# Kernel optimization log

Hardware: AMD Instinct MI355X
Metric: run time of the kernel (lower is better)

Reference implementation:

```python
import jax, jax.numpy as jnp
import numpy as np

NCHAR, NHID, NSTACK, STACK, DEPTH, T = 256, 2048, 32, 512, 4, 4096
TOP = 0  # top_of_stack


def _xavier(k, shape):
    fan_in, fan_out = shape[-1], shape[-2]
    std = (2.0 / (fan_in + fan_out)) ** 0.5
    return (jax.random.normal(k, shape) * std).astype(jnp.float32)


def setup_inputs() -> dict:
    key = jax.random.key(0)
    ks = jax.random.split(key, 7)
    in2hid_w = _xavier(ks[0], (NHID, NCHAR))
    hid2hid_w = _xavier(ks[1], (NHID, NHID))  # mod=2 -> xavier, not zeros
    hid2act_w = _xavier(ks[2], (NSTACK, 3, NHID))
    # init zero-masks: hid2stack rows below TOP+1 kept, rest zero; stack2hid cols >= DEPTH zero
    hid2stack_w = _xavier(ks[3], (NSTACK, STACK, NHID)).at[:, TOP + 1:, :].set(0.0)
    stack2hid_w = _xavier(ks[4], (NSTACK, NHID, STACK)).at[:, :, TOP + DEPTH:].set(0.0)
    hid2out_w = _xavier(ks[5], (NCHAR, NHID))
    tokens = jax.random.randint(ks[6], (T,), 0, NCHAR, dtype=jnp.int32)
    return dict(tokens=tokens, in2hid_w=in2hid_w, hid2hid_w=hid2hid_w,
                hid2act_w=hid2act_w, hid2stack_w=hid2stack_w,
                stack2hid_w=stack2hid_w, hid2out_w=hid2out_w)


def reference(tokens, in2hid_w, hid2hid_w, hid2act_w, hid2stack_w, stack2hid_w, hid2out_w):
    """Sequential StackRNN (mod=2, use_noop=True, soft actions) over T tokens.
    Shift-matrix matmuls replaced by equivalent O(n) rolls (push/pop/noop
    matrices with TOP=0 are exactly shift-down / shift-up / identity).
    Returns per-step output probabilities [T, NCHAR]."""
    neg_one_col = jnp.full((NSTACK, 1), -1.0, jnp.float32)

    def step(carry, x_t):
        hidden, stacks = carry  # [NHID], [NSTACK, STACK]
        # h = U x_t + sum_s P_s s_{t-1}[:depth] + R h_{t-1}
        h = in2hid_w[:, x_t]
        h = h + jnp.einsum('snd,sd->n', stack2hid_w[:, :, TOP:TOP + DEPTH],
                           stacks[:, TOP:TOP + DEPTH])
        h = h + hid2hid_w @ hidden
        h = jax.nn.sigmoid(h)
        # per-stack action distribution: [pop, push, noop]
        acts = jax.nn.softmax(jnp.einsum('san,n->sa', hid2act_w, h), axis=-1)
        pop_w, push_w, noop_w = acts[:, 0:1], acts[:, 1:2], acts[:, 2:3]
        # pushed top value (only row TOP of hid2stack is used)
        top_val = jax.nn.sigmoid(jnp.clip(hid2stack_w[:, TOP, :] @ h, -50.0, 50.0))  # [NSTACK]
        pushed = jnp.concatenate([top_val[:, None], stacks[:, :-1]], axis=1)
        popped = jnp.concatenate([stacks[:, 1:], neg_one_col], axis=1)
        new_stacks = push_w * pushed + pop_w * popped + noop_w * stacks
        probs = jax.nn.softmax(hid2out_w @ h)
        return (h, new_stacks), probs

    hidden0 = jnp.zeros((NHID,), jnp.float32)
    stacks0 = jnp.full((NSTACK, STACK), -1.0, jnp.float32)
    _, out = jax.lax.scan(step, (hidden0, stacks0), tokens)
    return out  # [T, NCHAR]
```

## Files before the change

kernel.cpp:

```cpp
#include <hip/hip_runtime.h>
#include <math.h>

#define NCHAR 256
#define NHID 2048
#define NSTACK 32
#define STACK 512
#define T 4096
#define NB 64
#define BT 1024
#define RPB 32
#define PROW 128
#define FPAD 16
#define AGENT __HIP_MEMORY_SCOPE_AGENT

__device__ __forceinline__ float cohLoadF(const float* p) {
  return __hip_atomic_load(p, __ATOMIC_RELAXED, AGENT);
}
__device__ __forceinline__ void cohStoreF(float* p, float v) {
  __hip_atomic_store(p, v, __ATOMIC_RELAXED, AGENT);
}
__device__ __forceinline__ float4 cohLoad4(const float4* p) {
  float4 r;
  asm volatile("global_load_dwordx4 %0, %1, off sc0 sc1\n\ts_waitcnt vmcnt(0)"
               : "=&v"(r) : "v"(p) : "memory");
  return r;
}
__device__ __forceinline__ void cohLoad4x4(const float4* p0, const float4* p1,
                                           const float4* p2, const float4* p3,
                                           float4& r0, float4& r1,
                                           float4& r2, float4& r3) {
  asm volatile(
      "global_load_dwordx4 %0, %4, off sc0 sc1\n\t"
      "global_load_dwordx4 %1, %5, off sc0 sc1\n\t"
      "global_load_dwordx4 %2, %6, off sc0 sc1\n\t"
      "global_load_dwordx4 %3, %7, off sc0 sc1\n\t"
      "s_waitcnt vmcnt(0)"
      : "=&v"(r0), "=&v"(r1), "=&v"(r2), "=&v"(r3)
      : "v"(p0), "v"(p1), "v"(p2), "v"(p3)
      : "memory");
}

__global__ __launch_bounds__(BT, 4) void stackrnn_seq(
    const int* __restrict__ tokens,
    const float* __restrict__ in2hid,
    const float* __restrict__ hid2hid,
    const float* __restrict__ hid2act,
    const float* __restrict__ hid2stack,
    const float* __restrict__ stack2hid,
    const float* __restrict__ hid2out,
    float* __restrict__ out,
    float* __restrict__ Hbuf,
    float* __restrict__ Pbuf,
    float* __restrict__ TopsG,
    int*   __restrict__ flags)
{
  __shared__ int    sTok[T];
  __shared__ float4 sH[576];
  __shared__ float4 sPq[32][17];
  __shared__ float  sLl[16][128];
  __shared__ float  sSt[2][STACK];
  __shared__ float  sHnew[RPB];
  __shared__ float  sActs[NSTACK][3];
  __shared__ float  sTopv[NSTACK];
  __shared__ float  sTops[NSTACK][4];
  __shared__ float  sOut[16];

  const int tid = threadIdx.x;
  const int b   = blockIdx.x;
  const int wv  = tid >> 6;
  const int l   = tid & 63;
  const int r0  = b * RPB + 2 * wv;
  const int r1  = r0 + 1;

  float wA[32], wB[32];
  {
    const float4* pa = (const float4*)(hid2hid + (size_t)r0 * NHID + 32 * l);
    const float4* pb = (const float4*)(hid2hid + (size_t)r1 * NHID + 32 * l);
#pragma unroll
    for (int j = 0; j < 8; ++j) {
      float4 v = pa[j];
      wA[4*j] = v.x; wA[4*j+1] = v.y; wA[4*j+2] = v.z; wA[4*j+3] = v.w;
    }
#pragma unroll
    for (int j = 0; j < 8; ++j) {
      float4 v = pb[j];
      wB[4*j] = v.x; wB[4*j+1] = v.y; wB[4*j+2] = v.z; wB[4*j+3] = v.w;
    }
  }
  float wl00, wl01, wl10, wl11;
  {
    const int g0 = 2 * l, g1 = 2 * l + 1;
    const int s0 = g0 >> 2, k0 = g0 & 3, s1 = g1 >> 2, k1 = g1 & 3;
    const float* p0 = (k0 < 3) ? (hid2act + (size_t)(3 * s0 + k0) * NHID)
                               : (hid2stack + (size_t)s0 * STACK * NHID);
    const float* p1 = (k1 < 3) ? (hid2act + (size_t)(3 * s1 + k1) * NHID)
                               : (hid2stack + (size_t)s1 * STACK * NHID);
    wl00 = p0[r0]; wl01 = p0[r1];
    wl10 = p1[r0]; wl11 = p1[r1];
  }
  const int cs = l >> 1, cd = (l & 1) * 2;
  float w2a0, w2a1, w2b0, w2b1;
  {
    const float* p = stack2hid + (size_t)cs * NHID * STACK;
    w2a0 = p[(size_t)r0 * STACK + cd]; w2a1 = p[(size_t)r0 * STACK + cd + 1];
    w2b0 = p[(size_t)r1 * STACK + cd]; w2b1 = p[(size_t)r1 * STACK + cd + 1];
  }
  const int oseg = wv >> 2;
  float wo[8];
  {
    const int ocol = 4 * b + (wv & 3);
    const float4* p = (const float4*)(hid2out + (size_t)ocol * NHID + oseg * 512 + 8 * l);
    float4 v0 = p[0], v1 = p[1];
    wo[0] = v0.x; wo[1] = v0.y; wo[2] = v0.z; wo[3] = v0.w;
    wo[4] = v1.x; wo[5] = v1.y; wo[6] = v1.z; wo[7] = v1.w;
  }

  for (int i = tid; i < T; i += BT) sTok[i] = tokens[i];
  float bval = -1.f;

  __syncthreads();

#pragma unroll 1
  for (int w = 0; w < T; ++w) {
    const int pw_ = w & 1, pr_ = pw_ ^ 1;
    const int xt  = sTok[w];
    const float e0 = in2hid[(size_t)r0 * NCHAR + xt];
    const float e1 = in2hid[(size_t)r1 * NCHAR + xt];

    if (w > 0 && wv == 0) {
      int v;
      do {
        v = __hip_atomic_load(&flags[l * FPAD], __ATOMIC_RELAXED, AGENT);
      } while (__any(v < w));
    }
    __syncthreads();

    float tg0 = -1.f, tg1 = -1.f, tg2 = -1.f, tg3 = -1.f, tg4 = -1.f;
    if (w > 0) {
      if (tid >= 512) {
        const int u = tid - 512;
        float4 hv = cohLoad4((const float4*)(Hbuf + (size_t)pr_ * NHID) + u);
        sH[u + (u >> 3)] = hv;
      } else {
        const int q = tid >> 4, bg = tid & 15;
        const float* base = Pbuf + (size_t)pr_ * NB * PROW + (size_t)(4 * bg) * PROW + 4 * q;
        float4 a0, a1, a2, a3;
        cohLoad4x4((const float4*)base, (const float4*)(base + PROW),
                   (const float4*)(base + 2 * PROW), (const float4*)(base + 3 * PROW),
                   a0, a1, a2, a3);
        float4 s4;
        s4.x = a0.x + a1.x + a2.x + a3.x;
        s4.y = a0.y + a1.y + a2.y + a3.y;
        s4.z = a0.z + a1.z + a2.z + a3.z;
        s4.w = a0.w + a1.w + a2.w + a3.w;
        sPq[q][bg] = s4;
        if (tid < NSTACK) {
          const float* tp = TopsG + ((size_t)pr_ * NSTACK + tid) * 16;
          tg0 = cohLoadF(tp);     tg1 = cohLoadF(tp + 1); tg2 = cohLoadF(tp + 2);
          tg3 = cohLoadF(tp + 3); tg4 = cohLoadF(tp + 4);
        }
      }
    }
    __syncthreads();

    if (tid < NSTACK) {
      if (w > 0) {
        float4 a = make_float4(0.f, 0.f, 0.f, 0.f);
#pragma unroll
        for (int g = 0; g < 16; ++g) {
          const float4 p = sPq[tid][(g + tid) & 15];
          a.x += p.x; a.y += p.y; a.z += p.z; a.w += p.w;
        }
        const float m  = fmaxf(a.x, fmaxf(a.y, a.z));
        const float ea = expf(a.x - m), eb = expf(a.y - m), ec = expf(a.z - m);
        const float inv = 1.f / (ea + eb + ec);
        const float qw = ea * inv, pwt = eb * inv, nw = ec * inv;
        sActs[tid][0] = qw; sActs[tid][1] = pwt; sActs[tid][2] = nw;
        float tv = fminf(50.f, fmaxf(-50.f, a.w));
        tv = 1.f / (1.f + expf(-tv));
        sTopv[tid] = tv;
        sTops[tid][0] = pwt * tv  + qw * tg1 + nw * tg0;
        sTops[tid][1] = pwt * tg0 + qw * tg2 + nw * tg1;
        sTops[tid][2] = pwt * tg1 + qw * tg3 + nw * tg2;
        sTops[tid][3] = pwt * tg2 + qw * tg4 + nw * tg3;
      } else {
        sActs[tid][0] = sActs[tid][1] = sActs[tid][2] = 0.f;
        sTopv[tid] = 0.f;
        sTops[tid][0] = sTops[tid][1] = sTops[tid][2] = sTops[tid][3] = -1.f;
      }
    }
    float acc0 = 0.f, acc1 = 0.f;
    if (w > 0) {
#pragma unroll
      for (int j = 0; j < 8; ++j) {
        const float4 hv = sH[9 * l + j];
        acc0 += wA[4*j]*hv.x + wA[4*j+1]*hv.y + wA[4*j+2]*hv.z + wA[4*j+3]*hv.w;
        acc1 += wB[4*j]*hv.x + wB[4*j+1]*hv.y + wB[4*j+2]*hv.z + wB[4*j+3]*hv.w;
      }
    }
    __syncthreads();

    acc0 += w2a0 * sTops[cs][cd] + w2a1 * sTops[cs][cd + 1];
    acc1 += w2b0 * sTops[cs][cd] + w2b1 * sTops[cs][cd + 1];
#pragma unroll
    for (int m = 1; m < 64; m <<= 1) {
      acc0 += __shfl_xor(acc0, m);
      acc1 += __shfl_xor(acc1, m);
    }
    const float h0 = 1.f / (1.f + expf(-(acc0 + e0)));
    const float h1 = 1.f / (1.f + expf(-(acc1 + e1)));
    if (l == 0) { sHnew[2 * wv] = h0; sHnew[2 * wv + 1] = h1; }
    *(float2*)&sLl[wv][2 * l] =
        make_float2(wl00 * h0 + wl01 * h1, wl10 * h0 + wl11 * h1);

    if (b < NSTACK && tid >= 512) {
      const int d = tid - 512;
      float nv;
      if (w > 0) {
        const float left   = (d > 0) ? sSt[pr_][d - 1] : 0.f;
        const float pushed = (d == 0) ? sTopv[b] : left;
        const float popped = (d < STACK - 1) ? sSt[pr_][d + 1] : -1.f;
        nv = sActs[b][1] * pushed + sActs[b][0] * popped + sActs[b][2] * bval;
      } else {
        nv = -1.f;
      }
      bval = nv;
      sSt[pw_][d] = nv;
      if (d < 5) cohStoreF(&TopsG[((size_t)pw_ * NSTACK + b) * 16 + d], nv);
    }
    if (w > 0) {
      const int f0 = oseg * 128 + 2 * l;
      const float4 hv0 = sH[f0 + (f0 >> 3)];
      const float4 hv1 = sH[(f0 + 1) + ((f0 + 1) >> 3)];
      float dv = wo[0]*hv0.x + wo[1]*hv0.y + wo[2]*hv0.z + wo[3]*hv0.w
               + wo[4]*hv1.x + wo[5]*hv1.y + wo[6]*hv1.z + wo[7]*hv1.w;
#pragma unroll
      for (int m = 1; m < 64; m <<= 1) dv += __shfl_xor(dv, m);
      if (l == 0) sOut[wv] = dv;
    }
    __syncthreads();

    if (tid < 128) {
      float pv = 0.f;
#pragma unroll
      for (int g = 0; g < 16; ++g) pv += sLl[g][tid];
      cohStoreF(&Pbuf[(size_t)pw_ * NB * PROW + (size_t)b * PROW + tid], pv);
    } else if (tid < 160) {
      cohStoreF(&Hbuf[(size_t)pw_ * NHID + b * RPB + (tid - 128)], sHnew[tid - 128]);
    }
    if (w > 0 && tid < 4)
      out[(size_t)(w - 1) * NCHAR + 4 * b + tid] =
          sOut[tid] + sOut[4 + tid] + sOut[8 + tid] + sOut[12 + tid];

    asm volatile("s_waitcnt vmcnt(0)" ::: "memory");
    __syncthreads();
    if (tid == 0)
      __hip_atomic_store(&flags[b * FPAD], w + 1, __ATOMIC_RELAXED, AGENT);
  }

  if (wv == 0) {
    int v;
    do {
      v = __hip_atomic_load(&flags[l * FPAD], __ATOMIC_RELAXED, AGENT);
    } while (__any(v < T));
  }
  __syncthreads();
  {
    const float* hb = Hbuf + (size_t)((T - 1) & 1) * NHID + oseg * 512 + 8 * l;
    float dv = 0.f;
#pragma unroll
    for (int e = 0; e < 8; ++e) dv += wo[e] * cohLoadF(hb + e);
#pragma unroll
    for (int m = 1; m < 64; m <<= 1) dv += __shfl_xor(dv, m);
    if (l == 0) sOut[wv] = dv;
  }
  __syncthreads();
  if (tid < 4)
    out[(size_t)(T - 1) * NCHAR + 4 * b + tid] =
        sOut[tid] + sOut[4 + tid] + sOut[8 + tid] + sOut[12 + tid];
}

__global__ __launch_bounds__(64) void row_softmax(float* __restrict__ out) {
  const int t = blockIdx.x;
  const int l = threadIdx.x;
  float4* p = (float4*)(out + (size_t)t * NCHAR);
  float4 v = p[l];
  float m = fmaxf(fmaxf(v.x, v.y), fmaxf(v.z, v.w));
#pragma unroll
  for (int k = 1; k < 64; k <<= 1) m = fmaxf(m, __shfl_xor(m, k));
  const float ex = expf(v.x - m), ey = expf(v.y - m);
  const float ez = expf(v.z - m), ew = expf(v.w - m);
  float s = ex + ey + ez + ew;
#pragma unroll
  for (int k = 1; k < 64; k <<= 1) s += __shfl_xor(s, k);
  const float inv = 1.f / s;
  p[l] = make_float4(ex * inv, ey * inv, ez * inv, ew * inv);
}

extern "C" void kernel_launch(void* const* d_in, const int* in_sizes, int n_in,
                              void* d_out, int out_size, void* d_ws, size_t ws_size,
                              hipStream_t stream) {
  const int*   tokens    = (const int*)d_in[0];
  const float* in2hid    = (const float*)d_in[1];
  const float* hid2hid   = (const float*)d_in[2];
  const float* hid2act   = (const float*)d_in[3];
  const float* hid2stack = (const float*)d_in[4];
  const float* stack2hid = (const float*)d_in[5];
  const float* hid2out   = (const float*)d_in[6];
  float* out = (float*)d_out;

  float* ws    = (float*)d_ws;
  float* Hbuf  = ws;
  float* Pbuf  = Hbuf + 2 * NHID;
  float* TopsG = Pbuf + 2 * NB * PROW;
  int*   flags = (int*)(TopsG + 1024);

  hipLaunchKernelGGL(stackrnn_seq, dim3(NB), dim3(BT), 0, stream,
                     tokens, in2hid, hid2hid, hid2act, hid2stack, stack2hid,
                     hid2out, out, Hbuf, Pbuf, TopsG, flags);
  hipLaunchKernelGGL(row_softmax, dim3(T), dim3(64), 0, stream, out);
}
```

Measured before the change: 33.49 ms.

## Replace per-block flag barrier with tagged value records in triple-buffered exchange

Each exchanged value (hidden state, partial action/stack sums, stack tops) is now written as a 64-bit record of the value plus a step tag, and consumers spin directly on the data until the tags match. This removes the per-step flag store, the vmcnt wait before it, the flag polling loop and one block barrier. The buffers become triple-buffered so a fast block cannot overwrite data a slow block still needs. The hid2out dot product also moves earlier in the step. In exchange, twice as many bytes cross the coherent fabric, and every consumer polls many addresses, which may raise memory traffic. The workspace must start without stale tags equal to the first expected step value.

```diff
diff --git a/kernel.cpp b/kernel.cpp
--- a/kernel.cpp
+++ b/kernel.cpp
@@ -9,38 +9,52 @@
 #define NB 64
 #define BT 1024
 #define RPB 32
-#define PROW 128
-#define FPAD 16
+#define HPP 2048
+#define PPP (64*128)
+#define TPP (32*8)
 #define AGENT __HIP_MEMORY_SCOPE_AGENT
 
-__device__ __forceinline__ float cohLoadF(const float* p) {
-  return __hip_atomic_load(p, __ATOMIC_RELAXED, AGENT);
-}
-__device__ __forceinline__ void cohStoreF(float* p, float v) {
-  __hip_atomic_store(p, v, __ATOMIC_RELAXED, AGENT);
-}
-__device__ __forceinline__ float4 cohLoad4(const float4* p) {
-  float4 r;
-  asm volatile("global_load_dwordx4 %0, %1, off sc0 sc1\n\ts_waitcnt vmcnt(0)"
-               : "=&v"(r) : "v"(p) : "memory");
-  return r;
-}
-__device__ __forceinline__ void cohLoad4x4(const float4* p0, const float4* p1,
-                                           const float4* p2, const float4* p3,
-                                           float4& r0, float4& r1,
-                                           float4& r2, float4& r3) {
+__device__ __forceinline__ void cohStoreRec(void* p, float v, float tag) {
+  unsigned long long u = (unsigned long long)__float_as_uint(v) |
+                         ((unsigned long long)__float_as_uint(tag) << 32);
+  __hip_atomic_store((unsigned long long*)p, u, __ATOMIC_RELAXED, AGENT);
+}
+__device__ __forceinline__ void cohLoad2x16(const void* p, float4& r0, float4& r1) {
   asm volatile(
-      "global_load_dwordx4 %0, %4, off sc0 sc1\n\t"
-      "global_load_dwordx4 %1, %5, off sc0 sc1\n\t"
-      "global_load_dwordx4 %2, %6, off sc0 sc1\n\t"
-      "global_load_dwordx4 %3, %7, off sc0 sc1\n\t"
+      "global_load_dwordx4 %0, %2, off sc0 sc1\n\t"
+      "global_load_dwordx4 %1, %2, off offset:16 sc0 sc1\n\t"
       "s_waitcnt vmcnt(0)"
-      : "=&v"(r0), "=&v"(r1), "=&v"(r2), "=&v"(r3)
-      : "v"(p0), "v"(p1), "v"(p2), "v"(p3)
-      : "memory");
-}
-
-__global__ __launch_bounds__(BT, 4) void stackrnn_seq(
+      : "=&v"(r0), "=&v"(r1) : "v"(p) : "memory");
+}
+__device__ __forceinline__ void cohLoad3x16(const void* p, float4& r0, float4& r1, float4& r2) {
+  asm volatile(
+      "global_load_dwordx4 %0, %3, off sc0 sc1\n\t"
+      "global_load_dwordx4 %1, %3, off offset:16 sc0 sc1\n\t"
+      "global_load_dwordx4 %2, %3, off offset:32 sc0 sc1\n\t"
+      "s_waitcnt vmcnt(0)"
+      : "=&v"(r0), "=&v"(r1), "=&v"(r2) : "v"(p) : "memory");
+}
+__device__ __forceinline__ void cohLoad8x16(const void* p,
+    float4& a0, float4& a1, float4& a2, float4& a3,
+    float4& a4, float4& a5, float4& a6, float4& a7) {
+  asm volatile(
+      "global_load_dwordx4 %0, %8, off sc0 sc1\n\t"
+      "global_load_dwordx4 %1, %8, off offset:16 sc0 sc1\n\t"
+      "global_load_dwordx4 %2, %8, off offset:1024 sc0 sc1\n\t"
+      "global_load_dwordx4 %3, %8, off offset:1040 sc0 sc1\n\t"
+      "global_load_dwordx4 %4, %8, off offset:2048 sc0 sc1\n\t"
+      "global_load_dwordx4 %5, %8, off offset:2064 sc0 sc1\n\t"
+      "global_load_dwordx4 %6, %8, off offset:3072 sc0 sc1\n\t"
+      "global_load_dwordx4 %7, %8, off offset:3088 sc0 sc1\n\t"
+      "s_waitcnt vmcnt(0)"
+      : "=&v"(a0), "=&v"(a1), "=&v"(a2), "=&v"(a3),
+        "=&v"(a4), "=&v"(a5), "=&v"(a6), "=&v"(a7)
+      : "v"(p) : "memory");
+}
+
+__global__ __launch_bounds__(BT, 4)
+__attribute__((amdgpu_waves_per_eu(4, 4)))
+void stackrnn_seq(
     const int* __restrict__ tokens,
     const float* __restrict__ in2hid,
     const float* __restrict__ hid2hid,
@@ -49,17 +63,15 @@
     const float* __restrict__ stack2hid,
     const float* __restrict__ hid2out,
     float* __restrict__ out,
-    float* __restrict__ Hbuf,
-    float* __restrict__ Pbuf,
-    float* __restrict__ TopsG,
-    int*   __restrict__ flags)
+    float2* __restrict__ HP,
+    float2* __restrict__ PP,
+    float2* __restrict__ TP)
 {
   __shared__ int    sTok[T];
   __shared__ float4 sH[576];
   __shared__ float4 sPq[32][17];
   __shared__ float  sLl[16][128];
   __shared__ float  sSt[2][STACK];
-  __shared__ float  sHnew[RPB];
   __shared__ float  sActs[NSTACK][3];
   __shared__ float  sTopv[NSTACK];
   __shared__ float  sTops[NSTACK][4];
@@ -122,43 +134,44 @@
 
 #pragma unroll 1
   for (int w = 0; w < T; ++w) {
-    const int pw_ = w & 1, pr_ = pw_ ^ 1;
-    const int xt  = sTok[w];
+    const int plc = (w + 2) % 3;
+    const int plp = w % 3;
+    const float tgc = (float)w;
+    const float tgp = (float)(w + 1);
+    const int xt = sTok[w];
     const float e0 = in2hid[(size_t)r0 * NCHAR + xt];
     const float e1 = in2hid[(size_t)r1 * NCHAR + xt];
 
-    if (w > 0 && wv == 0) {
-      int v;
-      do {
-        v = __hip_atomic_load(&flags[l * FPAD], __ATOMIC_RELAXED, AGENT);
-      } while (__any(v < w));
-    }
-    __syncthreads();
-
     float tg0 = -1.f, tg1 = -1.f, tg2 = -1.f, tg3 = -1.f, tg4 = -1.f;
     if (w > 0) {
-      if (tid >= 512) {
-        const int u = tid - 512;
-        float4 hv = cohLoad4((const float4*)(Hbuf + (size_t)pr_ * NHID) + u);
-        sH[u + (u >> 3)] = hv;
+      if (tid < 512) {
+        const float2* hp = HP + (size_t)plc * HPP + 4 * tid;
+        float4 x0, x1;
+        do { cohLoad2x16(hp, x0, x1); }
+        while (x0.y != tgc || x0.w != tgc || x1.y != tgc || x1.w != tgc);
+        sH[tid + (tid >> 3)] = make_float4(x0.x, x0.z, x1.x, x1.z);
+        if (tid < NSTACK) {
+          const float2* tp = TP + (size_t)plc * TPP + 8 * tid;
+          float4 t0, t1, t2;
+          do { cohLoad3x16(tp, t0, t1, t2); }
+          while (t0.y != tgc || t0.w != tgc || t1.y != tgc || t1.w != tgc || t2.y != tgc);
+          tg0 = t0.x; tg1 = t0.z; tg2 = t1.x; tg3 = t1.z; tg4 = t2.x;
+        }
       } else {
-        const int q = tid >> 4, bg = tid & 15;
-        const float* base = Pbuf + (size_t)pr_ * NB * PROW + (size_t)(4 * bg) * PROW + 4 * q;
-        float4 a0, a1, a2, a3;
-        cohLoad4x4((const float4*)base, (const float4*)(base + PROW),
-                   (const float4*)(base + 2 * PROW), (const float4*)(base + 3 * PROW),
-                   a0, a1, a2, a3);
+        const int v = tid - 512, q = v >> 4, bg = v & 15;
+        const float2* pp = PP + (size_t)plc * PPP + (size_t)(4 * bg) * 128 + 4 * q;
+        float4 a0, a1, a2, a3, a4, a5, a6, a7;
+        do { cohLoad8x16(pp, a0, a1, a2, a3, a4, a5, a6, a7); }
+        while (a0.y != tgc || a0.w != tgc || a1.y != tgc || a1.w != tgc ||
+               a2.y != tgc || a2.w != tgc || a3.y != tgc || a3.w != tgc ||
+               a4.y != tgc || a4.w != tgc || a5.y != tgc || a5.w != tgc ||
+               a6.y != tgc || a6.w != tgc || a7.y != tgc || a7.w != tgc);
         float4 s4;
-        s4.x = a0.x + a1.x + a2.x + a3.x;
-        s4.y = a0.y + a1.y + a2.y + a3.y;
-        s4.z = a0.z + a1.z + a2.z + a3.z;
-        s4.w = a0.w + a1.w + a2.w + a3.w;
+        s4.x = a0.x + a2.x + a4.x + a6.x;
+        s4.y = a0.z + a2.z + a4.z + a6.z;
+        s4.z = a1.x + a3.x + a5.x + a7.x;
+        s4.w = a1.z + a3.z + a5.z + a7.z;
         sPq[q][bg] = s4;
-        if (tid < NSTACK) {
-          const float* tp = TopsG + ((size_t)pr_ * NSTACK + tid) * 16;
-          tg0 = cohLoadF(tp);     tg1 = cohLoadF(tp + 1); tg2 = cohLoadF(tp + 2);
-          tg3 = cohLoadF(tp + 3); tg4 = cohLoadF(tp + 4);
-        }
       }
     }
     __syncthreads();
@@ -197,6 +210,14 @@
         acc0 += wA[4*j]*hv.x + wA[4*j+1]*hv.y + wA[4*j+2]*hv.z + wA[4*j+3]*hv.w;
         acc1 += wB[4*j]*hv.x + wB[4*j+1]*hv.y + wB[4*j+2]*hv.z + wB[4*j+3]*hv.w;
       }
+      const int f0 = oseg * 128 + 2 * l;
+      const float4 hv0 = sH[f0 + (f0 >> 3)];
+      const float4 hv1 = sH[(f0 + 1) + ((f0 + 1) >> 3)];
+      float dv = wo[0]*hv0.x + wo[1]*hv0.y + wo[2]*hv0.z + wo[3]*hv0.w
+               + wo[4]*hv1.x + wo[5]*hv1.y + wo[6]*hv1.z + wo[7]*hv1.w;
+#pragma unroll
+      for (int m = 1; m < 64; m <<= 1) dv += __shfl_xor(dv, m);
+      if (l == 0) sOut[wv] = dv;
     }
     __syncthreads();
 
@@ -209,12 +230,16 @@
     }
     const float h0 = 1.f / (1.f + expf(-(acc0 + e0)));
     const float h1 = 1.f / (1.f + expf(-(acc1 + e1)));
-    if (l == 0) { sHnew[2 * wv] = h0; sHnew[2 * wv + 1] = h1; }
+    if (l == 0) {
+      cohStoreRec(HP + (size_t)plp * HPP + r0, h0, tgp);
+      cohStoreRec(HP + (size_t)plp * HPP + r1, h1, tgp);
+    }
     *(float2*)&sLl[wv][2 * l] =
         make_float2(wl00 * h0 + wl01 * h1, wl10 * h0 + wl11 * h1);
 
     if (b < NSTACK && tid >= 512) {
       const int d = tid - 512;
+      const int pw_ = w & 1, pr_ = pw_ ^ 1;
       float nv;
       if (w > 0) {
         const float left   = (d > 0) ? sSt[pr_][d - 1] : 0.f;
@@ -226,58 +251,46 @@
       }
       bval = nv;
       sSt[pw_][d] = nv;
-      if (d < 5) cohStoreF(&TopsG[((size_t)pw_ * NSTACK + b) * 16 + d], nv);
-    }
-    if (w > 0) {
-      const int f0 = oseg * 128 + 2 * l;
-      const float4 hv0 = sH[f0 + (f0 >> 3)];
-      const float4 hv1 = sH[(f0 + 1) + ((f0 + 1) >> 3)];
-      float dv = wo[0]*hv0.x + wo[1]*hv0.y + wo[2]*hv0.z + wo[3]*hv0.w
-               + wo[4]*hv1.x + wo[5]*hv1.y + wo[6]*hv1.z + wo[7]*hv1.w;
-#pragma unroll
-      for (int m = 1; m < 64; m <<= 1) dv += __shfl_xor(dv, m);
-      if (l == 0) sOut[wv] = dv;
-    }
-    __syncthreads();
-
-    if (tid < 128) {
-      float pv = 0.f;
-#pragma unroll
-      for (int g = 0; g < 16; ++g) pv += sLl[g][tid];
-      cohStoreF(&Pbuf[(size_t)pw_ * NB * PROW + (size_t)b * PROW + tid], pv);
-    } else if (tid < 160) {
-      cohStoreF(&Hbuf[(size_t)pw_ * NHID + b * RPB + (tid - 128)], sHnew[tid - 128]);
+      if (d < 5)
+        cohStoreRec(TP + (size_t)plp * TPP + 8 * b + d, nv, tgp);
     }
     if (w > 0 && tid < 4)
       out[(size_t)(w - 1) * NCHAR + 4 * b + tid] =
           sOut[tid] + sOut[4 + tid] + sOut[8 + tid] + sOut[12 + tid];
-
-    asm volatile("s_waitcnt vmcnt(0)" ::: "memory");
-    __syncthreads();
-    if (tid == 0)
-      __hip_atomic_store(&flags[b * FPAD], w + 1, __ATOMIC_RELAXED, AGENT);
-  }
-
-  if (wv == 0) {
-    int v;
-    do {
-      v = __hip_atomic_load(&flags[l * FPAD], __ATOMIC_RELAXED, AGENT);
-    } while (__any(v < T));
-  }
-  __syncthreads();
-  {
-    const float* hb = Hbuf + (size_t)((T - 1) & 1) * NHID + oseg * 512 + 8 * l;
-    float dv = 0.f;
-#pragma unroll
-    for (int e = 0; e < 8; ++e) dv += wo[e] * cohLoadF(hb + e);
+    __syncthreads();
+
+    if (tid < 128) {
+      float pv = 0.f;
+#pragma unroll
+      for (int g = 0; g < 16; ++g) pv += sLl[g][tid];
+      cohStoreRec(PP + (size_t)plp * PPP + (size_t)b * 128 + tid, pv, tgp);
+    }
+  }
+
+  {
+    const int plc = (T - 1) % 3;
+    const float tgc = (float)T;
+    if (tid < 512) {
+      const float2* hp = HP + (size_t)plc * HPP + 4 * tid;
+      float4 x0, x1;
+      do { cohLoad2x16(hp, x0, x1); }
+      while (x0.y != tgc || x0.w != tgc || x1.y != tgc || x1.w != tgc);
+      sH[tid + (tid >> 3)] = make_float4(x0.x, x0.z, x1.x, x1.z);
+    }
+    __syncthreads();
+    const int f0 = oseg * 128 + 2 * l;
+    const float4 hv0 = sH[f0 + (f0 >> 3)];
+    const float4 hv1 = sH[(f0 + 1) + ((f0 + 1) >> 3)];
+    float dv = wo[0]*hv0.x + wo[1]*hv0.y + wo[2]*hv0.z + wo[3]*hv0.w
+             + wo[4]*hv1.x + wo[5]*hv1.y + wo[6]*hv1.z + wo[7]*hv1.w;
 #pragma unroll
     for (int m = 1; m < 64; m <<= 1) dv += __shfl_xor(dv, m);
     if (l == 0) sOut[wv] = dv;
-  }
-  __syncthreads();
-  if (tid < 4)
-    out[(size_t)(T - 1) * NCHAR + 4 * b + tid] =
-        sOut[tid] + sOut[4 + tid] + sOut[8 + tid] + sOut[12 + tid];
+    __syncthreads();
+    if (tid < 4)
+      out[(size_t)(T - 1) * NCHAR + 4 * b + tid] =
+          sOut[tid] + sOut[4 + tid] + sOut[8 + tid] + sOut[12 + tid];
+  }
 }
 
 __global__ __launch_bounds__(64) void row_softmax(float* __restrict__ out) {
@@ -309,14 +322,12 @@
   const float* hid2out   = (const float*)d_in[6];
   float* out = (float*)d_out;
 
-  float* ws    = (float*)d_ws;
-  float* Hbuf  = ws;
-  float* Pbuf  = Hbuf + 2 * NHID;
-  float* TopsG = Pbuf + 2 * NB * PROW;
-  int*   flags = (int*)(TopsG + 1024);
+  float2* HP = (float2*)d_ws;
+  float2* PP = HP + 3 * HPP;
+  float2* TP = PP + 3 * PPP;
 
   hipLaunchKernelGGL(stackrnn_seq, dim3(NB), dim3(BT), 0, stream,
                      tokens, in2hid, hid2hid, hid2act, hid2stack, stack2hid,
-                     hid2out, out, Hbuf, Pbuf, TopsG, flags);
+                     hid2out, out, HP, PP, TP);
   hipLaunchKernelGGL(row_softmax, dim3(T), dim3(64), 0, stream, out);
 }
```

Result: slower. 44.04 ms (+31.5%).
